# Kernel tuning notes

Measured on AMD Instinct MI355X. Metric: run time of the kernel, lower is better.

Reference implementation:

```python
import jax, jax.numpy as jnp
import numpy as np

# Segment boundaries from the original hard-coded slices: 13,13,13,9,4 repeated twice
SEG_BOUNDS = [0, 13, 26, 39, 48, 52, 65, 78, 91, 100, 104]


def segmented_log_softmax(x):
    # x: [B, 104]; independent log-softmax over each of the 10 fixed segments
    return jnp.concatenate(
        [jax.nn.log_softmax(x[:, a:b], axis=-1)
         for a, b in zip(SEG_BOUNDS[:-1], SEG_BOUNDS[1:])], axis=-1)


def setup_inputs() -> dict:
    key = jax.random.key(0)
    ks = jax.random.split(key, 8)
    B, H, D = 8192, 2048, 104
    return {
        "line": jax.random.normal(ks[0], (B, D), dtype=jnp.float32),
        "hidden": jax.random.normal(ks[1], (B, H), dtype=jnp.float32),
        "U_w": jax.random.normal(ks[2], (H, H), dtype=jnp.float32) * 0.02,
        "U_b": jax.random.normal(ks[3], (H,), dtype=jnp.float32) * 0.02,
        "W_w": jax.random.normal(ks[4], (H, D), dtype=jnp.float32) * 0.02,
        "W_b": jax.random.normal(ks[5], (H,), dtype=jnp.float32) * 0.02,
        "V_w": jax.random.normal(ks[6], (D, H), dtype=jnp.float32) * 0.02,
        "V_b": jax.random.normal(ks[7], (D,), dtype=jnp.float32) * 0.02,
    }


def reference(line, hidden, U_w, U_b, W_w, W_b, V_w, V_b):
    # h_t = sigmoid(U(hidden) + W(line)); torch Linear: y = x @ W.T + b
    h_t = jax.nn.sigmoid(hidden @ U_w.T + U_b + line @ W_w.T + W_b)  # [B, H]
    pred = h_t @ V_w.T + V_b                                          # [B, 104]
    pred_logsoft = segmented_log_softmax(pred)                        # [B, 104]
    return pred_logsoft, h_t
```

## Files before the change

### kernel.cpp

```cpp
#include <hip/hip_runtime.h>
#include <cstdint>
#include <cstddef>


typedef __bf16 bf16x8 __attribute__((ext_vector_type(8)));
typedef float  f32x4  __attribute__((ext_vector_type(4)));
typedef float  f32x16 __attribute__((ext_vector_type(16)));
typedef int    i32x4  __attribute__((ext_vector_type(4)));
typedef int    i32x8  __attribute__((ext_vector_type(8)));
typedef unsigned short ushort8 __attribute__((ext_vector_type(8)));
typedef unsigned char  uchar8  __attribute__((ext_vector_type(8)));
typedef float  float4v __attribute__((ext_vector_type(4)));

#define BB 8192
#define HH 2048
#define DD 104

static __device__ __forceinline__ unsigned short f2bf(float f) {
  unsigned u = __float_as_uint(f);
  unsigned r = (u + 0x7FFFu + ((u >> 16) & 1u)) >> 16;
  return (unsigned short)r;
}

static __device__ __forceinline__ unsigned char f2fp8(float x) {
  unsigned u = __float_as_uint(x);
  unsigned s = (u >> 24) & 0x80u;
  float ax = fabsf(x);
  ax = fminf(ax, 448.0f);
  unsigned code;
  if (ax >= 0.015625f) {
    unsigned b = __float_as_uint(ax);
    unsigned lsb = (b >> 20) & 1u;
    b += 0x0007FFFFu + lsb;
    unsigned e = (b >> 23) & 0xFFu;
    code = ((e - 120u) << 3) | ((b >> 20) & 7u);
  } else {
    code = (unsigned)__float2int_rn(ax * 512.0f);
  }
  return (unsigned char)(s | code);
}

#define GLD_LDS(g, l)                                                          \
  __builtin_amdgcn_global_load_lds(                                            \
      (__attribute__((address_space(1))) void*)(g),                            \
      (__attribute__((address_space(3))) void*)(l), 16, 0, 0)

#define MEMFENCE asm volatile("" ::: "memory")
#define MFMA16(a, b, c) __builtin_amdgcn_mfma_f32_16x16x32_bf16((a), (b), (c), 0, 0, 0)

__global__ __launch_bounds__(256) void conv_fp8_kernel(
    const float* __restrict__ hidden, const float* __restrict__ Uw,
    unsigned char* __restrict__ out_h, unsigned char* __restrict__ out_u) {
  long long i = ((long long)blockIdx.x * blockDim.x + threadIdx.x) * 8;
  const float* src; unsigned char* dst; long long off;
  if (i < (long long)BB * HH) { src = hidden; dst = out_h; off = i; }
  else { src = Uw; dst = out_u; off = i - (long long)BB * HH; }
  float4v a = *(const float4v*)(src + off);
  float4v b = *(const float4v*)(src + off + 4);
  uchar8 o;
  o[0]=f2fp8(a[0]); o[1]=f2fp8(a[1]); o[2]=f2fp8(a[2]); o[3]=f2fp8(a[3]);
  o[4]=f2fp8(b[0]); o[5]=f2fp8(b[1]); o[6]=f2fp8(b[2]); o[7]=f2fp8(b[3]);
  *(uchar8*)(dst + off) = o;
}

__global__ __launch_bounds__(256) void pad_mixed_kernel(
    const float* __restrict__ line, const float* __restrict__ Ww,
    const float* __restrict__ Vw,
    unsigned char* __restrict__ line8, unsigned char* __restrict__ Ww8,
    unsigned short* __restrict__ Vw_bf) {
  int i = blockIdx.x * blockDim.x + threadIdx.x;
  const int N1 = BB * 128;
  const int N2 = N1 + HH * 128;
  if (i < N1) {
    int r = i >> 7, c = i & 127;
    line8[i] = (c < DD) ? f2fp8(line[r * DD + c]) : (unsigned char)0;
  } else if (i < N2) {
    int j = i - N1; int r = j >> 7, c = j & 127;
    Ww8[j] = (c < DD) ? f2fp8(Ww[r * DD + c]) : (unsigned char)0;
  } else {
    int j = i - N2; int r = j >> 11, c = j & 2047;
    Vw_bf[j] = (r < DD) ? f2bf(Vw[r * 2048 + c]) : (unsigned short)0;
  }
}

static __device__ __forceinline__ i32x8 frd(const unsigned char* buf, int row, int pbase) {
  const unsigned char* p = buf + pbase * 2048 + row * 16;
  i32x4 lo = *(const i32x4*)(p);
  i32x4 hi = *(const i32x4*)(p + 2048);
  i32x8 r;
  r[0]=lo[0]; r[1]=lo[1]; r[2]=lo[2]; r[3]=lo[3];
  r[4]=hi[0]; r[5]=hi[1]; r[6]=hi[2]; r[7]=hi[3];
  return r;
}

__global__ __launch_bounds__(256, 2) void gemm1_kernel(
    const unsigned char* __restrict__ A8,
    const unsigned char* __restrict__ L8,
    const unsigned char* __restrict__ U8w,
    const unsigned char* __restrict__ W8w,
    const float* __restrict__ Ub, const float* __restrict__ Wb,
    float* __restrict__ outH, unsigned short* __restrict__ outHbf) {
  __shared__ __attribute__((aligned(16))) unsigned char smem[65536];
  const int t = threadIdx.x;
  const int l = t & 63;
  const int wid = t >> 6;
  const int wr = wid >> 1, wc = wid & 1;

  const int bid = blockIdx.x;
  const int wg = (bid & 7) * 128 + (bid >> 3);
  const int brow = (wg >> 4) * 128;
  const int bcol = (wg & 15) * 128;

  const int lr = l & 31;
  const int lc = l >> 5;

  const int sr = t & 127;
  const int sp = (t >> 7) * 16;
  const unsigned char* pA = A8 + (size_t)(brow + sr) * 2048 + sp;
  const unsigned char* pL = L8 + (size_t)(brow + sr) * 128 + sp;
  const unsigned char* pU = U8w + (size_t)(bcol + sr) * 2048 + sp;
  const unsigned char* pW = W8w + (size_t)(bcol + sr) * 128 + sp;
  unsigned char* dA = smem + t * 16;
  unsigned char* dB = smem + 32768 + t * 16;

  f32x16 acc[2][2] = {};

  auto stage = [&](int kt, int buf) {
    unsigned char* da = dA + buf * 16384;
    unsigned char* db = dB + buf * 16384;
    const int kb = kt * 128;
    if (kb < 2048) {
#pragma unroll
      for (int q = 0; q < 4; ++q) {
        GLD_LDS(pA + kb + q * 32, da + q * 4096);
        GLD_LDS(pU + kb + q * 32, db + q * 4096);
      }
    } else {
#pragma unroll
      for (int q = 0; q < 4; ++q) {
        GLD_LDS(pL + q * 32, da + q * 4096);
        GLD_LDS(pW + q * 32, db + q * 4096);
      }
    }
  };

  stage(0, 0);
  for (int kt = 0; kt < 17; ++kt) {
    const int cur = kt & 1;
    if (kt < 16) {
      stage(kt + 1, cur ^ 1);
      asm volatile("s_waitcnt vmcnt(8)" ::: "memory");
    } else {
      asm volatile("s_waitcnt vmcnt(0)" ::: "memory");
    }
    MEMFENCE; __builtin_amdgcn_s_barrier(); MEMFENCE;

    const unsigned char* Ab = smem + cur * 16384;
    const unsigned char* Bb = smem + 32768 + cur * 16384;
#pragma unroll
    for (int s = 0; s < 2; ++s) {
      const int pb = s * 4 + lc * 2;
      i32x8 af[2], bfv[2];
#pragma unroll
      for (int m = 0; m < 2; ++m) af[m] = frd(Ab, wr * 64 + m * 32 + lr, pb);
#pragma unroll
      for (int n = 0; n < 2; ++n) bfv[n] = frd(Bb, wc * 64 + n * 32 + lr, pb);
      __builtin_amdgcn_s_setprio(1);
#pragma unroll
      for (int m = 0; m < 2; ++m)
#pragma unroll
        for (int n = 0; n < 2; ++n)
          acc[m][n] = __builtin_amdgcn_mfma_scale_f32_32x32x64_f8f6f4(
              af[m], bfv[n], acc[m][n], 0 , 0 ,
              0, 0x7F7F7F7F , 0, 0x7F7F7F7F );
      __builtin_amdgcn_s_setprio(0);
    }
    MEMFENCE; __builtin_amdgcn_s_barrier(); MEMFENCE;
  }

#pragma unroll
  for (int nf = 0; nf < 2; ++nf) {
    const int col = bcol + wc * 64 + nf * 32 + lr;
    const float bias = Ub[col] + Wb[col];
#pragma unroll
    for (int mf = 0; mf < 2; ++mf) {
#pragma unroll
      for (int reg = 0; reg < 16; ++reg) {
        const int row = brow + wr * 64 + mf * 32 + (reg & 3) + 8 * (reg >> 2) + 4 * lc;
        const float v = acc[mf][nf][reg] + bias;
        const float h = 1.0f / (1.0f + __expf(-v));
        const size_t idx = (size_t)row * HH + col;
        outH[idx] = h;
        outHbf[idx] = f2bf(h);
      }
    }
  }
}

template <int NM, int NN>
static __device__ __forceinline__ void mfma_step(
    const unsigned short* sA, const unsigned short* sB, int arow0, int brow0,
    int frow, int fk, f32x4 (&acc)[NM][NN]) {
  bf16x8 af[NM], bfr[NN];
#pragma unroll
  for (int m = 0; m < NM; ++m)
    af[m] = *(const bf16x8*)(sA + (arow0 + m * 16 + frow) * 32 + fk);
#pragma unroll
  for (int n = 0; n < NN; ++n)
    bfr[n] = *(const bf16x8*)(sB + (brow0 + n * 16 + frow) * 32 + fk);
#pragma unroll
  for (int m = 0; m < NM; ++m)
#pragma unroll
    for (int n = 0; n < NN; ++n)
      acc[m][n] = MFMA16(af[m], bfr[n], acc[m][n]);
}

__global__ __launch_bounds__(256, 2) void gemm2_kernel(
    const unsigned short* __restrict__ A,
    const unsigned short* __restrict__ Bm,
    const float* __restrict__ Vb,
    float* __restrict__ outLS) {
  __shared__ unsigned short sA[64 * 32];
  __shared__ unsigned short sB[128 * 32];
  __shared__ float pred[64 * 105];
  const int t = threadIdx.x;
  const int l = t & 63;
  const int wid = t >> 6, wr = wid >> 1, wc = wid & 1;
  const int brow = blockIdx.x * 64;
  const int srow = t >> 2, scg = t & 3;
  const int frow = l & 15, fk = (l >> 4) * 8;

  const unsigned short* gA = A + (size_t)(brow + srow) * HH + scg * 8;
  const unsigned short* gB = Bm + (size_t)srow * HH + scg * 8;
  unsigned short* lA = sA + t * 8;
  unsigned short* lB = sB + t * 8;

  f32x4 acc[2][4] = {};
  for (int ks = 0; ks < 64; ++ks) {
    __syncthreads();
    GLD_LDS(gA, lA);
    GLD_LDS(gB, lB);
    GLD_LDS(gB + 64 * HH, lB + 64 * 32);
    gA += 32; gB += 32;
    __syncthreads();
    mfma_step<2, 4>(sA, sB, wr * 32, wc * 64, frow, fk, acc);
  }

#pragma unroll
  for (int n = 0; n < 4; ++n) {
    const int col = wc * 64 + n * 16 + frow;
    if (col < DD) {
      const float vb = Vb[col];
#pragma unroll
      for (int m = 0; m < 2; ++m) {
        const int r0 = wr * 32 + m * 16 + (l >> 4) * 4;
#pragma unroll
        for (int j = 0; j < 4; ++j)
          pred[(r0 + j) * 105 + col] = acc[m][n][j] + vb;
      }
    }
  }
  __syncthreads();

  if (t < 64) {
    const int segb[11] = {0, 13, 26, 39, 48, 52, 65, 78, 91, 100, 104};
    const float* p = pred + t * 105;
    float* o = outLS + (size_t)(brow + t) * DD;
    for (int s = 0; s < 10; ++s) {
      const int a = segb[s], b = segb[s + 1];
      float mx = -3.0e38f;
      for (int c = a; c < b; ++c) mx = fmaxf(mx, p[c]);
      float sum = 0.0f;
      for (int c = a; c < b; ++c) sum += __expf(p[c] - mx);
      const float ls = __logf(sum) + mx;
      for (int c = a; c < b; ++c) o[c] = p[c] - ls;
    }
  }
}

extern "C" void kernel_launch(void* const* d_in, const int* in_sizes, int n_in,
                              void* d_out, int out_size, void* d_ws, size_t ws_size,
                              hipStream_t stream) {
  (void)in_sizes; (void)n_in; (void)out_size; (void)ws_size;
  const float* line   = (const float*)d_in[0];
  const float* hidden = (const float*)d_in[1];
  const float* Uw     = (const float*)d_in[2];
  const float* Ub     = (const float*)d_in[3];
  const float* Ww     = (const float*)d_in[4];
  const float* Wb     = (const float*)d_in[5];
  const float* Vw     = (const float*)d_in[6];
  const float* Vb     = (const float*)d_in[7];

  char* ws = (char*)d_ws;
  unsigned char* hid8    = (unsigned char*)(ws);
  unsigned char* U8w     = (unsigned char*)(ws + 16777216);
  unsigned char* line8   = (unsigned char*)(ws + 20971520);
  unsigned char* Ww8     = (unsigned char*)(ws + 22020096);
  unsigned short* Vw_bf  = (unsigned short*)(ws + 22282240);
  unsigned short* ht_bf  = (unsigned short*)(ws + 22806528);

  float* outLS = (float*)d_out;
  float* outH  = (float*)d_out + (size_t)BB * DD;

  conv_fp8_kernel<<<10240, 256, 0, stream>>>(hidden, Uw, hid8, U8w);
  pad_mixed_kernel<<<6144, 256, 0, stream>>>(line, Ww, Vw, line8, Ww8, Vw_bf);
  gemm1_kernel<<<1024, 256, 0, stream>>>(hid8, line8, U8w, Ww8, Ub, Wb,
                                         outH, ht_bf);
  gemm2_kernel<<<128, 256, 0, stream>>>(ht_bf, Vw_bf, Vb, outLS);
}
```

Baseline: 140.8 us.

## Use 8 waves per gemm1 block and halve gemm2 row tile

gemm1 now runs 512 threads (8 waves in a 2x4 grid), with each wave computing a 64x32 output slice instead of 64x64, and each thread staging half as many global-to-LDS loads. gemm2 processes 32 rows per block instead of 64, doubling the grid to 256 blocks so more CUs are busy for the small second GEMM and the log-softmax. The aim is more latency hiding in gemm1 and better CU coverage in gemm2. In exchange, each wave does less MFMA work per LDS fragment read, gemm2 blocks re-load the shared V weights more times, and launch_bounds(512,4) may restrict registers per thread.

After: 140.5 us. Within noise of the previous version (-0.2%).

```diff
diff --git a/kernel.cpp b/kernel.cpp
--- a/kernel.cpp
+++ b/kernel.cpp
@@ -93,7 +93,7 @@
   return r;
 }
 
-__global__ __launch_bounds__(256, 2) void gemm1_kernel(
+__global__ __launch_bounds__(512, 4) void gemm1_kernel(
     const unsigned char* __restrict__ A8,
     const unsigned char* __restrict__ L8,
     const unsigned char* __restrict__ U8w,
@@ -104,7 +104,7 @@
   const int t = threadIdx.x;
   const int l = t & 63;
   const int wid = t >> 6;
-  const int wr = wid >> 1, wc = wid & 1;
+  const int wr = wid >> 2, wc = wid & 3;
 
   const int bid = blockIdx.x;
   const int wg = (bid & 7) * 128 + (bid >> 3);
@@ -123,7 +123,7 @@
   unsigned char* dA = smem + t * 16;
   unsigned char* dB = smem + 32768 + t * 16;
 
-  f32x16 acc[2][2] = {};
+  f32x16 acc[2] = {};
 
   auto stage = [&](int kt, int buf) {
     unsigned char* da = dA + buf * 16384;
@@ -131,15 +131,15 @@
     const int kb = kt * 128;
     if (kb < 2048) {
 #pragma unroll
-      for (int q = 0; q < 4; ++q) {
-        GLD_LDS(pA + kb + q * 32, da + q * 4096);
-        GLD_LDS(pU + kb + q * 32, db + q * 4096);
+      for (int q = 0; q < 2; ++q) {
+        GLD_LDS(pA + kb + q * 64, da + q * 8192);
+        GLD_LDS(pU + kb + q * 64, db + q * 8192);
       }
     } else {
 #pragma unroll
-      for (int q = 0; q < 4; ++q) {
-        GLD_LDS(pL + q * 32, da + q * 4096);
-        GLD_LDS(pW + q * 32, db + q * 4096);
+      for (int q = 0; q < 2; ++q) {
+        GLD_LDS(pL + q * 64, da + q * 8192);
+        GLD_LDS(pW + q * 64, db + q * 8192);
       }
     }
   };
@@ -149,7 +149,7 @@
     const int cur = kt & 1;
     if (kt < 16) {
       stage(kt + 1, cur ^ 1);
-      asm volatile("s_waitcnt vmcnt(8)" ::: "memory");
+      asm volatile("s_waitcnt vmcnt(4)" ::: "memory");
     } else {
       asm volatile("s_waitcnt vmcnt(0)" ::: "memory");
     }
@@ -160,34 +160,28 @@
 #pragma unroll
     for (int s = 0; s < 2; ++s) {
       const int pb = s * 4 + lc * 2;
-      i32x8 af[2], bfv[2];
-#pragma unroll
-      for (int m = 0; m < 2; ++m) af[m] = frd(Ab, wr * 64 + m * 32 + lr, pb);
-#pragma unroll
-      for (int n = 0; n < 2; ++n) bfv[n] = frd(Bb, wc * 64 + n * 32 + lr, pb);
+      i32x8 af0 = frd(Ab, wr * 64 + lr, pb);
+      i32x8 af1 = frd(Ab, wr * 64 + 32 + lr, pb);
+      i32x8 bf_ = frd(Bb, wc * 32 + lr, pb);
       __builtin_amdgcn_s_setprio(1);
-#pragma unroll
-      for (int m = 0; m < 2; ++m)
-#pragma unroll
-        for (int n = 0; n < 2; ++n)
-          acc[m][n] = __builtin_amdgcn_mfma_scale_f32_32x32x64_f8f6f4(
-              af[m], bfv[n], acc[m][n], 0 , 0 ,
-              0, 0x7F7F7F7F , 0, 0x7F7F7F7F );
+      acc[0] = __builtin_amdgcn_mfma_scale_f32_32x32x64_f8f6f4(
+          af0, bf_, acc[0], 0, 0, 0, 0x7F7F7F7F, 0, 0x7F7F7F7F);
+      acc[1] = __builtin_amdgcn_mfma_scale_f32_32x32x64_f8f6f4(
+          af1, bf_, acc[1], 0, 0, 0, 0x7F7F7F7F, 0, 0x7F7F7F7F);
       __builtin_amdgcn_s_setprio(0);
     }
     MEMFENCE; __builtin_amdgcn_s_barrier(); MEMFENCE;
   }
 
-#pragma unroll
-  for (int nf = 0; nf < 2; ++nf) {
-    const int col = bcol + wc * 64 + nf * 32 + lr;
+  {
+    const int col = bcol + wc * 32 + lr;
     const float bias = Ub[col] + Wb[col];
 #pragma unroll
     for (int mf = 0; mf < 2; ++mf) {
 #pragma unroll
       for (int reg = 0; reg < 16; ++reg) {
         const int row = brow + wr * 64 + mf * 32 + (reg & 3) + 8 * (reg >> 2) + 4 * lc;
-        const float v = acc[mf][nf][reg] + bias;
+        const float v = acc[mf][reg] + bias;
         const float h = 1.0f / (1.0f + __expf(-v));
         const size_t idx = (size_t)row * HH + col;
         outH[idx] = h;
@@ -220,30 +214,30 @@
     const unsigned short* __restrict__ Bm,
     const float* __restrict__ Vb,
     float* __restrict__ outLS) {
-  __shared__ unsigned short sA[64 * 32];
+  __shared__ unsigned short sA[32 * 32];
   __shared__ unsigned short sB[128 * 32];
-  __shared__ float pred[64 * 105];
+  __shared__ float pred[32 * 105];
   const int t = threadIdx.x;
   const int l = t & 63;
   const int wid = t >> 6, wr = wid >> 1, wc = wid & 1;
-  const int brow = blockIdx.x * 64;
+  const int brow = blockIdx.x * 32;
   const int srow = t >> 2, scg = t & 3;
   const int frow = l & 15, fk = (l >> 4) * 8;
 
-  const unsigned short* gA = A + (size_t)(brow + srow) * HH + scg * 8;
+  const unsigned short* gA = A + (size_t)(brow + (t >> 2 & 31)) * HH + scg * 8;
   const unsigned short* gB = Bm + (size_t)srow * HH + scg * 8;
   unsigned short* lA = sA + t * 8;
   unsigned short* lB = sB + t * 8;
 
-  f32x4 acc[2][4] = {};
+  f32x4 acc[1][4] = {};
   for (int ks = 0; ks < 64; ++ks) {
     __syncthreads();
-    GLD_LDS(gA, lA);
+    if (t < 128) GLD_LDS(gA, lA);
     GLD_LDS(gB, lB);
     GLD_LDS(gB + 64 * HH, lB + 64 * 32);
     gA += 32; gB += 32;
     __syncthreads();
-    mfma_step<2, 4>(sA, sB, wr * 32, wc * 64, frow, fk, acc);
+    mfma_step<1, 4>(sA, sB, wr * 16, wc * 64, frow, fk, acc);
   }
 
 #pragma unroll
@@ -251,18 +245,15 @@
     const int col = wc * 64 + n * 16 + frow;
     if (col < DD) {
       const float vb = Vb[col];
-#pragma unroll
-      for (int m = 0; m < 2; ++m) {
-        const int r0 = wr * 32 + m * 16 + (l >> 4) * 4;
-#pragma unroll
-        for (int j = 0; j < 4; ++j)
-          pred[(r0 + j) * 105 + col] = acc[m][n][j] + vb;
-      }
+      const int r0 = wr * 16 + (l >> 4) * 4;
+#pragma unroll
+      for (int j = 0; j < 4; ++j)
+        pred[(r0 + j) * 105 + col] = acc[0][n][j] + vb;
     }
   }
   __syncthreads();
 
-  if (t < 64) {
+  if (t < 32) {
     const int segb[11] = {0, 13, 26, 39, 48, 52, 65, 78, 91, 100, 104};
     const float* p = pred + t * 105;
     float* o = outLS + (size_t)(brow + t) * DD;
@@ -304,7 +295,7 @@
 
   conv_fp8_kernel<<<10240, 256, 0, stream>>>(hidden, Uw, hid8, U8w);
   pad_mixed_kernel<<<6144, 256, 0, stream>>>(line, Ww, Vw, line8, Ww8, Vw_bf);
-  gemm1_kernel<<<1024, 256, 0, stream>>>(hid8, line8, U8w, Ww8, Ub, Wb,
+  gemm1_kernel<<<1024, 512, 0, stream>>>(hid8, line8, U8w, Ww8, Ub, Wb,
                                          outH, ht_bf);
-  gemm2_kernel<<<128, 256, 0, stream>>>(ht_bf, Vw_bf, Vb, outLS);
-}
+  gemm2_kernel<<<256, 256, 0, stream>>>(ht_bf, Vw_bf, Vb, outLS);
+}
```
